# Kernel tuning notes

Hardware: AMD Instinct MI355X
Metric: run time of the kernel (lower is better)

The kernel has to match this reference:

```python
import jax, jax.numpy as jnp
import numpy as np
import math

N, T, D_MODEL = 4, 2048, 1024
NHEAD = 16
HEAD_DIM = D_MODEL // NHEAD
ROTARY_DIM = 64
WINDOW = (128, 128)
ROPE_BASE = 10000.0


def _rope_cos_sin(seq_len, rotary_dim, dtype):
    # non-interleaved (GPT-NeoX style) rotary embedding tables
    inv_freq = 1.0 / (ROPE_BASE ** (jnp.arange(0, rotary_dim, 2, dtype=jnp.float32) / rotary_dim))
    t = jnp.arange(seq_len, dtype=jnp.float32)
    freqs = jnp.outer(t, inv_freq)  # [T, rotary_dim//2]
    return jnp.cos(freqs).astype(dtype), jnp.sin(freqs).astype(dtype)


def _apply_rope(x, cos, sin):
    # x: [N, T, H, D]; rotate first ROTARY_DIM dims, pass the rest through
    r = ROTARY_DIM
    x_rot, x_pass = x[..., :r], x[..., r:]
    x1, x2 = x_rot[..., : r // 2], x_rot[..., r // 2 :]
    c = cos[None, :, None, :]
    s = sin[None, :, None, :]
    out = jnp.concatenate([x1 * c - x2 * s, x1 * s + x2 * c], axis=-1)
    return jnp.concatenate([out, x_pass], axis=-1)


def _sliding_window_bias(seq_len, window, dtype):
    i = jnp.arange(seq_len)[:, None]
    j = jnp.arange(seq_len)[None, :]
    # triu(diag=-w0) & tril(diag=w1): keep j - i in [-w0, w1]
    keep = (j - i >= -window[0]) & (j - i <= window[1])
    return jnp.where(keep, jnp.zeros((), dtype), jnp.full((), -jnp.inf, dtype))


def setup_inputs() -> dict:
    key = jax.random.key(0)
    k1, k2, k3 = jax.random.split(key, 3)
    x = jax.random.normal(k1, (N, T, D_MODEL), dtype=jnp.float32)
    Wqkv = jax.random.normal(k2, (D_MODEL, 3 * D_MODEL), dtype=jnp.float32) * (1.0 / math.sqrt(D_MODEL))
    Wout = jax.random.normal(k3, (D_MODEL, D_MODEL), dtype=jnp.float32) * (1.0 / math.sqrt(D_MODEL))
    bout = jnp.zeros((D_MODEL,), dtype=jnp.float32)
    return {"x": x, "Wqkv": Wqkv, "Wout": Wout, "bout": bout}


def reference(x, Wqkv, Wout, bout):
    n, t, _ = x.shape
    qkv = (x @ Wqkv).reshape(n, t, 3, NHEAD, HEAD_DIM)
    q, k, v = qkv[:, :, 0], qkv[:, :, 1], qkv[:, :, 2]  # each [N, T, H, D]
    cos, sin = _rope_cos_sin(t, ROTARY_DIM, x.dtype)
    q = _apply_rope(q, cos, sin)
    k = _apply_rope(k, cos, sin)
    scale = 1.0 / math.sqrt(HEAD_DIM)
    bias = _sliding_window_bias(t, WINDOW, x.dtype)  # [T, T]
    scores = jnp.einsum("bthd,bshd->bhts", q, k) * scale + bias[None, None]
    attn = jax.nn.softmax(scores, axis=-1)
    out = jnp.einsum("bhts,bshd->bthd", attn, v).reshape(n, t, D_MODEL)
    return out @ Wout + bout
```

## Files before the change

kernel.cpp:

```cpp
#include <hip/hip_runtime.h>
#include <hip/hip_bf16.h>
#include <cstdint>
#include <cstddef>

typedef __bf16 bf16_t;
typedef bf16_t bf16x8 __attribute__((ext_vector_type(8)));
typedef float f32x4 __attribute__((ext_vector_type(4)));
typedef unsigned short ushort_t;

#define T_SEQ 2048
#define DM 1024
#define NH 16
#define HD 64
#define WIN 128
#define ROPE_C 0.28782313662425572f
#define SCALE_LOG2E 0.18033688011112042f
#define ATT_M 16.0f

__device__ __forceinline__ ushort_t f2bf(float f) {
    union { float f; unsigned u; } v; v.f = f;
    unsigned r = v.u + 0x7fff + ((v.u >> 16) & 1);
    return (ushort_t)(r >> 16);
}
__device__ __forceinline__ float sane(float v, float sent) {
    return (fabsf(v) < 1e30f) ? v : sent;
}
__device__ __forceinline__ void gld16(const ushort_t* g, ushort_t* l) {
    __builtin_amdgcn_global_load_lds(
        (const __attribute__((address_space(1))) unsigned int*)g,
        (__attribute__((address_space(3))) unsigned int*)l, 16, 0, 0);
}

__global__ __launch_bounds__(256) void kzero_f(float* __restrict__ p) {
    size_t i = ((size_t)blockIdx.x * 256 + threadIdx.x) * 4;
    float4 z; z.x = z.y = z.z = z.w = 0.f;
    *(float4*)(p + i) = z;
}

__device__ __forceinline__ void trans_f2b_tile(const float* __restrict__ in,
                                               ushort_t* __restrict__ out,
                                               int R, int C, int c0, int r0) {
    __shared__ __align__(16) ushort_t tile[64][72];
    const int tid = threadIdx.x;
    const int rl = tid >> 2, q4 = tid & 3;
    const float* src = in + (size_t)(r0 + rl) * C + c0 + q4 * 16;
    ushort_t cv[16];
#pragma unroll
    for (int i = 0; i < 4; i++) {
        float4 f = *(const float4*)(src + i * 4);
        cv[i * 4 + 0] = f2bf(f.x); cv[i * 4 + 1] = f2bf(f.y);
        cv[i * 4 + 2] = f2bf(f.z); cv[i * 4 + 3] = f2bf(f.w);
    }
    *(uint4*)&tile[rl][q4 * 16]     = *(uint4*)&cv[0];
    *(uint4*)&tile[rl][q4 * 16 + 8] = *(uint4*)&cv[8];
    __syncthreads();
    const int cl = tid >> 2;
    ushort_t tmp[16];
#pragma unroll
    for (int i = 0; i < 16; i++) tmp[i] = tile[q4 * 16 + i][cl];
    ushort_t* dst = out + (size_t)(c0 + cl) * R + r0 + q4 * 16;
    *(uint4*)(dst)     = *(uint4*)&tmp[0];
    *(uint4*)(dst + 8) = *(uint4*)&tmp[8];
}

__global__ __launch_bounds__(256) void prep(const float* __restrict__ x,
                                            const float* __restrict__ Wqkv,
                                            const float* __restrict__ Wout,
                                            ushort_t* __restrict__ xb,
                                            ushort_t* __restrict__ WqkvT,
                                            ushort_t* __restrict__ WoutT) {
    const int bx = blockIdx.x;
    if (bx < 4096) {
        size_t i = ((size_t)bx * 256 + threadIdx.x) * 8;
        float4 a0 = *(const float4*)(x + i);
        float4 a1 = *(const float4*)(x + i + 4);
        ushort_t cv[8];
        cv[0] = f2bf(a0.x); cv[1] = f2bf(a0.y); cv[2] = f2bf(a0.z); cv[3] = f2bf(a0.w);
        cv[4] = f2bf(a1.x); cv[5] = f2bf(a1.y); cv[6] = f2bf(a1.z); cv[7] = f2bf(a1.w);
        *(uint4*)(xb + i) = *(uint4*)cv;
    } else if (bx < 4864) {
        int tb = bx - 4096;
        trans_f2b_tile(Wqkv, WqkvT, 1024, 3072, (tb % 48) * 64, (tb / 48) * 64);
    } else {
        int tb = bx - 4864;
        trans_f2b_tile(Wout, WoutT, 1024, 1024, (tb & 15) * 64, (tb >> 4) * 64);
    }
}

#define BM 128
#define BN 256
#define BK 32
#define KTILES 32
#define LBUF ((BM + BN) * BK)
#define LTOT (3 * LBUF)

__device__ __forceinline__ void gemm_core(const ushort_t* __restrict__ Agl,
                                          const ushort_t* __restrict__ Bgl,
                                          ushort_t* L, int m0, int n0,
                                          f32x4 (&acc)[8][4]) {
    const int tid = threadIdx.x;
    const int lane = tid & 63, w = tid >> 6;
    const int c = lane & 15, g = lane >> 4;
    const int sv   = (lane & 7) ^ (lane >> 3);
    const int grow = 2 * (lane >> 3) + (sv >> 2);
    const int gcol = (sv & 3) * 8;
    const int loff = (c >> 1) * 64 + (((((c & 1) << 2) | g) ^ ((c >> 1) & 7)) * 8);

#pragma unroll
    for (int mi = 0; mi < 8; ++mi)
#pragma unroll
        for (int ni = 0; ni < 4; ++ni)
#pragma unroll
            for (int r = 0; r < 4; ++r) acc[mi][ni][r] = 0.f;

    auto STAGE = [&](int kt, int bo) {
        const int k0 = kt * BK;
#pragma unroll
        for (int j = 0; j < 2; ++j) {
            const ushort_t* ga = Agl + (size_t)(m0 + 32 * w + 16 * j + grow) * 1024 + k0 + gcol;
            gld16(ga, &L[bo + (w * 2 + j) * 512]);
        }
#pragma unroll
        for (int j = 0; j < 4; ++j) {
            const ushort_t* gb = Bgl + (size_t)(n0 + 64 * w + 16 * j + grow) * 1024 + k0 + gcol;
            gld16(gb, &L[bo + BM * BK + (w * 4 + j) * 512]);
        }
    };

    STAGE(0, 0);
    STAGE(1, LBUF);
    asm volatile("s_waitcnt vmcnt(6)\n\ts_barrier" ::: "memory");

    int bcur = 0;
    for (int kt = 0; kt < KTILES; ++kt) {
        int bst = bcur + 2 * LBUF; if (bst >= LTOT) bst -= LTOT;
        if (kt + 2 < KTILES) STAGE(kt + 2, bst);

        const ushort_t* La = L + bcur;
        const ushort_t* Bb = La + BM * BK;
        bf16x8 bfr[4], af0[4], af1[4];
#pragma unroll
        for (int ni = 0; ni < 4; ++ni)
            bfr[ni] = *(const bf16x8*)&Bb[w * 2048 + ni * 512 + loff];
#pragma unroll
        for (int mi = 0; mi < 4; ++mi)
            af0[mi] = *(const bf16x8*)&La[mi * 512 + loff];
        __builtin_amdgcn_s_setprio(1);
#pragma unroll
        for (int mi = 0; mi < 4; ++mi)
#pragma unroll
            for (int ni = 0; ni < 4; ++ni)
                acc[mi][ni] = __builtin_amdgcn_mfma_f32_16x16x32_bf16(
                    af0[mi], bfr[ni], acc[mi][ni], 0, 0, 0);
        __builtin_amdgcn_s_setprio(0);
#pragma unroll
    for (int mi = 0; mi < 4; ++mi)
            af1[mi] = *(const bf16x8*)&La[(mi + 4) * 512 + loff];
        __builtin_amdgcn_s_setprio(1);
#pragma unroll
        for (int mi = 0; mi < 4; ++mi)
#pragma unroll
            for (int ni = 0; ni < 4; ++ni)
                acc[mi + 4][ni] = __builtin_amdgcn_mfma_f32_16x16x32_bf16(
                    af1[mi], bfr[ni], acc[mi + 4][ni], 0, 0, 0);
        __builtin_amdgcn_s_setprio(0);
        if (kt < KTILES - 2)
            asm volatile("s_waitcnt vmcnt(6)\n\ts_barrier" ::: "memory");
        else if (kt == KTILES - 2)
            asm volatile("s_waitcnt vmcnt(0)\n\ts_barrier" ::: "memory");
        bcur += LBUF; if (bcur == LTOT) bcur = 0;
    }
}

__global__ __launch_bounds__(256, 2) void gemm_qkv(const ushort_t* __restrict__ A,
                                                   const ushort_t* __restrict__ Bt,
                                                   ushort_t* __restrict__ Qr,
                                                   ushort_t* __restrict__ Kr,
                                                   ushort_t* __restrict__ Vt) {
    __shared__ __align__(16) ushort_t L[LTOT];
    const int id  = blockIdx.x;
    const int nid = (id & 7) * 96 + (id >> 3);
    const int m0 = (nid & 63) * BM, n0 = (nid >> 6) * BN;
    f32x4 acc[8][4];
    gemm_core(A, Bt, L, m0, n0, acc);

    const int lane = threadIdx.x & 63, w = threadIdx.x >> 6;
    const int c = lane & 15, g = lane >> 4;
    const int nb = n0 + w * 64;
    const int sec = nb >> 10;
    const int h = (nb >> 6) & 15;

    if (sec < 2) {
        ushort_t* dst = (sec == 0) ? Qr : Kr;
        const float invf0 = __expf(-(float)(c) * ROPE_C);
        const float invf1 = __expf(-(float)(16 + c) * ROPE_C);
#pragma unroll
        for (int mi = 0; mi < 8; ++mi)
#pragma unroll
            for (int r = 0; r < 4; ++r) {
                int tg = m0 + mi * 16 + g * 4 + r;
                int nB = tg >> 11, t = tg & (T_SEQ - 1);
                float a0 = (float)t * invf0, a1 = (float)t * invf1;
                float s0 = __sinf(a0), c0 = __cosf(a0);
                float s1 = __sinf(a1), c1 = __cosf(a1);
                size_t base = ((size_t)(nB * NH + h) * T_SEQ + t) * 64;
                float x1a = acc[mi][0][r], x2a = acc[mi][2][r];
                float x1b = acc[mi][1][r], x2b = acc[mi][3][r];
                dst[base + c]      = f2bf(sane(x1a * c0 - x2a * s0, 1e3f));
                dst[base + 16 + c] = f2bf(sane(x1b * c1 - x2b * s1, 1e3f));
                dst[base + 32 + c] = f2bf(sane(x1a * s0 + x2a * c0, 1e3f));
                dst[base + 48 + c] = f2bf(sane(x1b * s1 + x2b * c1, 1e3f));
            }
    } else {
#pragma unroll
        for (int mi = 0; mi < 8; ++mi) {
            int tgb = m0 + mi * 16 + g * 4;
            int nB = tgb >> 11, t = tgb & (T_SEQ - 1);
            size_t vrow = (size_t)(nB * NH + h) * 64 * T_SEQ;
#pragma unroll
            for (int ni = 0; ni < 4; ++ni) {
                ushort4 pk;
                pk.x = f2bf(sane(acc[mi][ni][0], 1e3f));
                pk.y = f2bf(sane(acc[mi][ni][1], 1e3f));
                pk.z = f2bf(sane(acc[mi][ni][2], 1e3f));
                pk.w = f2bf(sane(acc[mi][ni][3], 1e3f));
                *(ushort4*)&Vt[vrow + (size_t)(ni * 16 + c) * T_SEQ + t] = pk;
            }
        }
    }
}

__global__ __launch_bounds__(256, 2) void gemm_out(const ushort_t* __restrict__ A,
                                                   const ushort_t* __restrict__ Bt,
                                                   float* __restrict__ C,
                                                   const float* __restrict__ bias) {
    __shared__ __align__(16) ushort_t L[LTOT];
    const int id  = blockIdx.x;
    const int nid = (id & 7) * 32 + (id >> 3);
    const int m0 = (nid & 63) * BM, n0 = (nid >> 6) * BN;
    f32x4 acc[8][4];
    gemm_core(A, Bt, L, m0, n0, acc);

    const int lane = threadIdx.x & 63, w = threadIdx.x >> 6;
    const int c = lane & 15, g = lane >> 4;
#pragma unroll
    for (int ni = 0; ni < 4; ++ni) {
        int col = n0 + w * 64 + ni * 16 + c;
        float bv = bias[col];
#pragma unroll
        for (int mi = 0; mi < 8; ++mi)
#pragma unroll
            for (int r = 0; r < 4; ++r) {
                int rowi = m0 + mi * 16 + g * 4 + r;
                C[(size_t)rowi * 1024 + col] = sane(acc[mi][ni][r] + bv, 1e8f);
            }
    }
}

#define KVB 64

__global__ __launch_bounds__(256) void attn_swin(const ushort_t* __restrict__ Qr,
                                                 const ushort_t* __restrict__ Kr,
                                                 const ushort_t* __restrict__ Vt,
                                                 ushort_t* __restrict__ O) {
    __shared__ __align__(16) ushort_t Ks[KVB * 72];
    __shared__ __align__(16) ushort_t Vs[64 * 72];
    __shared__ __align__(16) ushort_t pbuf[4][2][16 * 72];
    const int tid = threadIdx.x;
    const int wid = tid >> 6, lane = tid & 63;
    const int qb = (blockIdx.x & 15) * 128;
    const int h = (blockIdx.x >> 4) & 15, n = blockIdx.x >> 8;
    const int c = lane & 15, g = lane >> 4;
    const size_t hb = ((size_t)(n * NH + h)) * T_SEQ * 64;
    const int t0s[2] = { qb + wid * 16, qb + 64 + wid * 16 };
    const int st_row = tid >> 2, st_col = (tid & 3) * 16;

    bf16x8 qf0[2], qf1[2];
#pragma unroll
    for (int sub = 0; sub < 2; sub++) {
        qf0[sub] = *(const bf16x8*)(Qr + hb + (size_t)(t0s[sub] + c) * 64 + g * 8);
        qf1[sub] = *(const bf16x8*)(Qr + hb + (size_t)(t0s[sub] + c) * 64 + 32 + g * 8);
    }

    f32x4 o[2][4];
    float l_r[2][4];
#pragma unroll
    for (int sub = 0; sub < 2; sub++)
#pragma unroll
        for (int i = 0; i < 4; i++) {
            l_r[sub][i] = 0.f;
#pragma unroll
            for (int r = 0; r < 4; r++) o[sub][i][r] = 0.f;
        }

    int sB_lo = qb - WIN;        if (sB_lo < 0) sB_lo = 0;
    int sB_hi = qb + 127 + WIN;  if (sB_hi > T_SEQ - 1) sB_hi = T_SEQ - 1;

    uint4 kreg0 = *(const uint4*)(Kr + hb + (size_t)(sB_lo + st_row) * 64 + st_col);
    uint4 kreg1 = *(const uint4*)(Kr + hb + (size_t)(sB_lo + st_row) * 64 + st_col + 8);
    uint4 vreg0 = *(const uint4*)(Vt + hb + (size_t)st_row * T_SEQ + sB_lo + st_col);
    uint4 vreg1 = *(const uint4*)(Vt + hb + (size_t)st_row * T_SEQ + sB_lo + st_col + 8);

    for (int s0 = sB_lo; s0 <= sB_hi; s0 += KVB) {
        __syncthreads();
        *(uint4*)&Ks[st_row * 72 + st_col]     = kreg0;
        *(uint4*)&Ks[st_row * 72 + st_col + 8] = kreg1;
        *(uint4*)&Vs[st_row * 72 + st_col]     = vreg0;
        *(uint4*)&Vs[st_row * 72 + st_col + 8] = vreg1;
        __syncthreads();
        int s1 = s0 + KVB;
        if (s1 + KVB - 1 <= sB_hi) {
            kreg0 = *(const uint4*)(Kr + hb + (size_t)(s1 + st_row) * 64 + st_col);
            kreg1 = *(const uint4*)(Kr + hb + (size_t)(s1 + st_row) * 64 + st_col + 8);
            vreg0 = *(const uint4*)(Vt + hb + (size_t)st_row * T_SEQ + s1 + st_col);
            vreg1 = *(const uint4*)(Vt + hb + (size_t)st_row * T_SEQ + s1 + st_col + 8);
        }
        bool act[2];
#pragma unroll
        for (int sub = 0; sub < 2; sub++)
            act[sub] = !(s0 > t0s[sub] + 15 + WIN || s0 + KVB - 1 < t0s[sub] - WIN);
        if (!act[0] && !act[1]) continue;

        bf16x8 kf0[4], kf1[4];
#pragma unroll
        for (int sh = 0; sh < 4; sh++) {
            kf0[sh] = *(const bf16x8*)&Ks[(sh * 16 + c) * 72 + g * 8];
            kf1[sh] = *(const bf16x8*)&Ks[(sh * 16 + c) * 72 + 32 + g * 8];
        }
        bf16x8 vfl[4], vfh[4];
#pragma unroll
        for (int di = 0; di < 4; di++) {
            vfl[di] = *(const bf16x8*)&Vs[(di * 16 + c) * 72 + g * 8];
            vfh[di] = *(const bf16x8*)&Vs[(di * 16 + c) * 72 + 32 + g * 8];
        }

#pragma unroll
        for (int sub = 0; sub < 2; sub++) {
            if (!act[sub]) continue;
            const int t0 = t0s[sub];
            f32x4 S[4];
#pragma unroll
            for (int sh = 0; sh < 4; sh++) {
                f32x4 z;
#pragma unroll
                for (int r = 0; r < 4; r++) z[r] = 0.f;
                z = __builtin_amdgcn_mfma_f32_16x16x32_bf16(qf0[sub], kf0[sh], z, 0, 0, 0);
                z = __builtin_amdgcn_mfma_f32_16x16x32_bf16(qf1[sub], kf1[sh], z, 0, 0, 0);
                S[sh] = z;
            }
            const bool interior = (s0 >= t0 - 113) && (s0 <= t0 + 65);
            ushort_t* pb = pbuf[wid][sub];
            if (interior) {
#pragma unroll
                for (int sh = 0; sh < 4; sh++)
#pragma unroll
                    for (int r = 0; r < 4; r++) {
                        float p = exp2f(S[sh][r] * SCALE_LOG2E - ATT_M);
                        l_r[sub][r] += p;
                        pb[(g * 4 + r) * 72 + sh * 16 + c] = f2bf(p);
                    }
            } else {
#pragma unroll
                for (int sh = 0; sh < 4; sh++)
#pragma unroll
                    for (int r = 0; r < 4; r++) {
                        int s = s0 + sh * 16 + c;
                        int q = t0 + g * 4 + r;
                        bool keep = (s - q >= -WIN) && (s - q <= WIN);
                        float v = keep ? S[sh][r] * SCALE_LOG2E : -1e30f;
                        float p = exp2f(v - ATT_M);
                        l_r[sub][r] += p;
                        pb[(g * 4 + r) * 72 + sh * 16 + c] = f2bf(p);
                    }
            }
        }
        __asm__ volatile("s_waitcnt lgkmcnt(0)" ::: "memory");
#pragma unroll
        for (int sub = 0; sub < 2; sub++) {
            if (!act[sub]) continue;
            bf16x8 pfl = *(const bf16x8*)&pbuf[wid][sub][c * 72 + g * 8];
            bf16x8 pfh = *(const bf16x8*)&pbuf[wid][sub][c * 72 + 32 + g * 8];
#pragma unroll
            for (int di = 0; di < 4; di++) {
                o[sub][di] = __builtin_amdgcn_mfma_f32_16x16x32_bf16(pfl, vfl[di], o[sub][di], 0, 0, 0);
                o[sub][di] = __builtin_amdgcn_mfma_f32_16x16x32_bf16(pfh, vfh[di], o[sub][di], 0, 0, 0);
            }
        }
        __asm__ volatile("" ::: "memory");
    }

#pragma unroll
    for (int sub = 0; sub < 2; sub++) {
#pragma unroll
        for (int off = 1; off < 16; off <<= 1)
#pragma unroll
            for (int r = 0; r < 4; r++)
                l_r[sub][r] += __shfl_xor(l_r[sub][r], off, 64);
        float inv[4];
#pragma unroll
        for (int r = 0; r < 4; r++) inv[r] = __builtin_amdgcn_rcpf(l_r[sub][r]);
#pragma unroll
        for (int di = 0; di < 4; di++)
#pragma unroll
            for (int r = 0; r < 4; r++) {
                int q = t0s[sub] + g * 4 + r;
                float val = o[sub][di][r] * inv[r];
                O[((size_t)(n * T_SEQ + q)) * DM + h * 64 + di * 16 + c] =
                    f2bf(sane(val, 1e6f));
            }
    }
}

extern "C" void kernel_launch(void* const* d_in, const int* in_sizes, int n_in,
                              void* d_out, int out_size, void* d_ws, size_t ws_size,
                              hipStream_t stream) {
    const float* x    = (const float*)d_in[0];
    const float* Wqkv = (const float*)d_in[1];
    const float* Wout = (const float*)d_in[2];
    const float* bout = (const float*)d_in[3];
    float* out = (float*)d_out;

    const size_t NEED = 72ull << 20;
    if (ws_size < NEED) {
        kzero_f<<<dim3(8192), 256, 0, stream>>>(out);
        return;
    }
    char* ws = (char*)d_ws;
    ushort_t* WqkvT = (ushort_t*)(ws);
    ushort_t* WoutT = (ushort_t*)(ws + (6ull << 20));
    ushort_t* Qr    = (ushort_t*)(ws + (8ull << 20));
    ushort_t* Kr    = (ushort_t*)(ws + (24ull << 20));
    ushort_t* Vt    = (ushort_t*)(ws + (40ull << 20));
    ushort_t* xb    = (ushort_t*)(ws + (56ull << 20));
    ushort_t* Oat   = xb;

    prep<<<dim3(5120), 256, 0, stream>>>(x, Wqkv, Wout, xb, WqkvT, WoutT);
    gemm_qkv<<<dim3(768), 256, 0, stream>>>(xb, WqkvT, Qr, Kr, Vt);
    attn_swin<<<dim3(1024), 256, 0, stream>>>(Qr, Kr, Vt, Oat);
    gemm_out<<<dim3(256), 256, 0, stream>>>(Oat, WoutT, out, bout);
}
```

Measured before the change: 219.1 us.

## Use 256x128 tiles for output GEMM and drop block swizzle in GEMMs

Adds a second GEMM core with a 128-wide N tile and uses it for the output projection, doubling its grid from 256 to 512 blocks and raising occupancy hints to 3 blocks per CU. This targets poor CU utilisation, since 256 blocks underfill the device. Both GEMMs also switch from a swizzled 1D block index to a plain 2D grid, which may change L2 reuse patterns. Smaller N tiles lower arithmetic intensity and increase A-matrix reloads.

```diff
diff --git a/kernel.cpp b/kernel.cpp
--- a/kernel.cpp
+++ b/kernel.cpp
@@ -154,7 +154,7 @@
                     af0[mi], bfr[ni], acc[mi][ni], 0, 0, 0);
         __builtin_amdgcn_s_setprio(0);
 #pragma unroll
-    for (int mi = 0; mi < 4; ++mi)
+        for (int mi = 0; mi < 4; ++mi)
             af1[mi] = *(const bf16x8*)&La[(mi + 4) * 512 + loff];
         __builtin_amdgcn_s_setprio(1);
 #pragma unroll
@@ -172,15 +172,95 @@
     }
 }
 
+#define BN2 128
+#define LBUF2 ((BM + BN2) * BK)
+#define LTOT2 (3 * LBUF2)
+
+__device__ __forceinline__ void gemm_core_n128(const ushort_t* __restrict__ Agl,
+                                               const ushort_t* __restrict__ Bgl,
+                                               ushort_t* L, int m0, int n0,
+                                               f32x4 (&acc)[8][2]) {
+    const int tid = threadIdx.x;
+    const int lane = tid & 63, w = tid >> 6;
+    const int c = lane & 15, g = lane >> 4;
+    const int sv   = (lane & 7) ^ (lane >> 3);
+    const int grow = 2 * (lane >> 3) + (sv >> 2);
+    const int gcol = (sv & 3) * 8;
+    const int loff = (c >> 1) * 64 + (((((c & 1) << 2) | g) ^ ((c >> 1) & 7)) * 8);
+
+#pragma unroll
+    for (int mi = 0; mi < 8; ++mi)
+#pragma unroll
+        for (int ni = 0; ni < 2; ++ni)
+#pragma unroll
+            for (int r = 0; r < 4; ++r) acc[mi][ni][r] = 0.f;
+
+    auto STAGE = [&](int kt, int bo) {
+        const int k0 = kt * BK;
+#pragma unroll
+        for (int j = 0; j < 2; ++j) {
+            const ushort_t* ga = Agl + (size_t)(m0 + 32 * w + 16 * j + grow) * 1024 + k0 + gcol;
+            gld16(ga, &L[bo + (w * 2 + j) * 512]);
+        }
+#pragma unroll
+        for (int j = 0; j < 2; ++j) {
+            const ushort_t* gb = Bgl + (size_t)(n0 + 32 * w + 16 * j + grow) * 1024 + k0 + gcol;
+            gld16(gb, &L[bo + BM * BK + (w * 2 + j) * 512]);
+        }
+    };
+
+    STAGE(0, 0);
+    STAGE(1, LBUF2);
+    asm volatile("s_waitcnt vmcnt(4)\n\ts_barrier" ::: "memory");
+
+    int bcur = 0;
+    for (int kt = 0; kt < KTILES; ++kt) {
+        int bst = bcur + 2 * LBUF2; if (bst >= LTOT2) bst -= LTOT2;
+        if (kt + 2 < KTILES) STAGE(kt + 2, bst);
+
+        const ushort_t* La = L + bcur;
+        const ushort_t* Bb = La + BM * BK;
+        bf16x8 bfr[2], af0[4], af1[4];
+#pragma unroll
+        for (int ni = 0; ni < 2; ++ni)
+            bfr[ni] = *(const bf16x8*)&Bb[w * 1024 + ni * 512 + loff];
+#pragma unroll
+        for (int mi = 0; mi < 4; ++mi)
+            af0[mi] = *(const bf16x8*)&La[mi * 512 + loff];
+        __builtin_amdgcn_s_setprio(1);
+#pragma unroll
+        for (int mi = 0; mi < 4; ++mi)
+#pragma unroll
+            for (int ni = 0; ni < 2; ++ni)
+                acc[mi][ni] = __builtin_amdgcn_mfma_f32_16x16x32_bf16(
+                    af0[mi], bfr[ni], acc[mi][ni], 0, 0, 0);
+        __builtin_amdgcn_s_setprio(0);
+#pragma unroll
+        for (int mi = 0; mi < 4; ++mi)
+            af1[mi] = *(const bf16x8*)&La[(mi + 4) * 512 + loff];
+        __builtin_amdgcn_s_setprio(1);
+#pragma unroll
+        for (int mi = 0; mi < 4; ++mi)
+#pragma unroll
+            for (int ni = 0; ni < 2; ++ni)
+                acc[mi + 4][ni] = __builtin_amdgcn_mfma_f32_16x16x32_bf16(
+                    af1[mi], bfr[ni], acc[mi + 4][ni], 0, 0, 0);
+        __builtin_amdgcn_s_setprio(0);
+        if (kt < KTILES - 2)
+            asm volatile("s_waitcnt vmcnt(4)\n\ts_barrier" ::: "memory");
+        else if (kt == KTILES - 2)
+            asm volatile("s_waitcnt vmcnt(0)\n\ts_barrier" ::: "memory");
+        bcur += LBUF2; if (bcur == LTOT2) bcur = 0;
+    }
+}
+
 __global__ __launch_bounds__(256, 2) void gemm_qkv(const ushort_t* __restrict__ A,
                                                    const ushort_t* __restrict__ Bt,
                                                    ushort_t* __restrict__ Qr,
                                                    ushort_t* __restrict__ Kr,
                                                    ushort_t* __restrict__ Vt) {
     __shared__ __align__(16) ushort_t L[LTOT];
-    const int id  = blockIdx.x;
-    const int nid = (id & 7) * 96 + (id >> 3);
-    const int m0 = (nid & 63) * BM, n0 = (nid >> 6) * BN;
+    const int m0 = blockIdx.x * BM, n0 = blockIdx.y * BN;
     f32x4 acc[8][4];
     gemm_core(A, Bt, L, m0, n0, acc);
 
@@ -230,22 +310,20 @@
     }
 }
 
-__global__ __launch_bounds__(256, 2) void gemm_out(const ushort_t* __restrict__ A,
+__global__ __launch_bounds__(256, 3) void gemm_out(const ushort_t* __restrict__ A,
                                                    const ushort_t* __restrict__ Bt,
                                                    float* __restrict__ C,
                                                    const float* __restrict__ bias) {
-    __shared__ __align__(16) ushort_t L[LTOT];
-    const int id  = blockIdx.x;
-    const int nid = (id & 7) * 32 + (id >> 3);
-    const int m0 = (nid & 63) * BM, n0 = (nid >> 6) * BN;
-    f32x4 acc[8][4];
-    gemm_core(A, Bt, L, m0, n0, acc);
+    __shared__ __align__(16) ushort_t L[LTOT2];
+    const int m0 = blockIdx.x * BM, n0 = blockIdx.y * BN2;
+    f32x4 acc[8][2];
+    gemm_core_n128(A, Bt, L, m0, n0, acc);
 
     const int lane = threadIdx.x & 63, w = threadIdx.x >> 6;
     const int c = lane & 15, g = lane >> 4;
 #pragma unroll
-    for (int ni = 0; ni < 4; ++ni) {
-        int col = n0 + w * 64 + ni * 16 + c;
+    for (int ni = 0; ni < 2; ++ni) {
+        int col = n0 + w * 32 + ni * 16 + c;
         float bv = bias[col];
 #pragma unroll
         for (int mi = 0; mi < 8; ++mi)
@@ -435,7 +513,7 @@
     ushort_t* Oat   = xb;
 
     prep<<<dim3(5120), 256, 0, stream>>>(x, Wqkv, Wout, xb, WqkvT, WoutT);
-    gemm_qkv<<<dim3(768), 256, 0, stream>>>(xb, WqkvT, Qr, Kr, Vt);
+    gemm_qkv<<<dim3(64, 12), 256, 0, stream>>>(xb, WqkvT, Qr, Kr, Vt);
     attn_swin<<<dim3(1024), 256, 0, stream>>>(Qr, Kr, Vt, Oat);
-    gemm_out<<<dim3(256), 256, 0, stream>>>(Oat, WoutT, out, bout);
-}
+    gemm_out<<<dim3(64, 8), 256, 0, stream>>>(Oat, WoutT, out, bout);
+}
```

Result: no change. 214.8 us (-2.0%).

## Use 256x256 eight-wave tiled GEMM with staged LDS pipeline for QKV projection

Applied to the files above, without the earlier changes.

Replaces the QKV projection GEMM with a 512-thread, 256x256-tile kernel that uses a BK=64 double-buffered LDS scheme. Global loads of A and B halves are interleaved between four MFMA phases, each fenced by barriers. The larger tile is meant to raise arithmetic intensity and cut global/L2 traffic per FLOP. The grid shrinks to 384 blocks of 512 threads, which gives fewer waves to fill the CUs and adds many barriers per k-step. The out-projection also drops its grouped block-index swizzle in favour of a plain 2D grid, which may hurt L2 locality.

```diff
diff --git a/kernel.cpp b/kernel.cpp
--- a/kernel.cpp
+++ b/kernel.cpp
@@ -87,6 +87,202 @@
     }
 }
 
+#define QDB 32768
+
+__device__ __forceinline__ void gemm8_core(const ushort_t* __restrict__ Agl,
+                                           const ushort_t* __restrict__ Bgl,
+                                           ushort_t* L, int m0, int n0,
+                                           f32x4 (&acc)[8][4]) {
+    const int tid = threadIdx.x;
+    const int lane = tid & 63, w = tid >> 6;
+    const int wr = w >> 2, wc = w & 3;
+    const int c = lane & 15, g = lane >> 4;
+    const int srow = lane >> 3;
+    const int gcol = ((lane & 7) ^ srow) * 8;
+    const int cx0 = ((0 + g) ^ (c & 7)) * 8;
+    const int cx1 = ((4 + g) ^ (c & 7)) * 8;
+    const int axb = wr * 8192;
+    const int bxb = 16384 + (wc >> 1) * 8192;
+    const int br0 = (wc & 1) * 64;
+
+#pragma unroll
+    for (int mi = 0; mi < 8; ++mi)
+#pragma unroll
+        for (int ni = 0; ni < 4; ++ni)
+#pragma unroll
+            for (int r = 0; r < 4; ++r) acc[mi][ni][r] = 0.f;
+
+    auto SHALF = [&](const ushort_t* G, int grow0, int kt, ushort_t* lbase) {
+#pragma unroll
+        for (int j = 0; j < 2; ++j)
+            gld16(G + (size_t)(grow0 + w * 16 + j * 8 + srow) * 1024 + kt * 64 + gcol,
+                  lbase + (w * 2 + j) * 512);
+    };
+
+    SHALF(Agl, m0,       0, L);
+    SHALF(Agl, m0 + 128, 0, L + 8192);
+    SHALF(Bgl, n0,       0, L + 16384);
+    SHALF(Bgl, n0 + 128, 0, L + 24576);
+    SHALF(Bgl, n0,       1, L + QDB + 16384);
+    SHALF(Bgl, n0 + 128, 1, L + QDB + 24576);
+    asm volatile("s_waitcnt vmcnt(4)\n\ts_barrier" ::: "memory");
+
+    bf16x8 afr[4][2], b0[2][2], b1[2][2];
+    int bc = 0;
+    for (int j = 0; j < 16; ++j) {
+        ushort_t* cur = L + bc;
+        ushort_t* nxt = L + (bc ^ QDB);
+
+#pragma unroll
+        for (int mi = 0; mi < 4; ++mi) {
+            const ushort_t* p = cur + axb + (mi * 16 + c) * 64;
+            afr[mi][0] = *(const bf16x8*)(p + cx0);
+            afr[mi][1] = *(const bf16x8*)(p + cx1);
+        }
+#pragma unroll
+        for (int ni = 0; ni < 2; ++ni) {
+            const ushort_t* p = cur + bxb + (br0 + ni * 16 + c) * 64;
+            b0[ni][0] = *(const bf16x8*)(p + cx0);
+            b0[ni][1] = *(const bf16x8*)(p + cx1);
+        }
+        if (j < 15) SHALF(Agl, m0, j + 1, nxt);
+        asm volatile("s_barrier\n\ts_waitcnt lgkmcnt(0)" ::: "memory");
+        __builtin_amdgcn_s_setprio(1);
+#pragma unroll
+        for (int mi = 0; mi < 4; ++mi)
+#pragma unroll
+            for (int ni = 0; ni < 2; ++ni) {
+                acc[mi][ni] = __builtin_amdgcn_mfma_f32_16x16x32_bf16(
+                    afr[mi][0], b0[ni][0], acc[mi][ni], 0, 0, 0);
+                acc[mi][ni] = __builtin_amdgcn_mfma_f32_16x16x32_bf16(
+                    afr[mi][1], b0[ni][1], acc[mi][ni], 0, 0, 0);
+            }
+        __builtin_amdgcn_s_setprio(0);
+        asm volatile("s_barrier" ::: "memory");
+
+#pragma unroll
+        for (int ni = 0; ni < 2; ++ni) {
+            const ushort_t* p = cur + bxb + (br0 + (ni + 2) * 16 + c) * 64;
+            b1[ni][0] = *(const bf16x8*)(p + cx0);
+            b1[ni][1] = *(const bf16x8*)(p + cx1);
+        }
+        if (j < 15) SHALF(Agl, m0 + 128, j + 1, nxt + 8192);
+        asm volatile("s_barrier\n\ts_waitcnt lgkmcnt(0)" ::: "memory");
+        __builtin_amdgcn_s_setprio(1);
+#pragma unroll
+        for (int mi = 0; mi < 4; ++mi)
+#pragma unroll
+            for (int ni = 0; ni < 2; ++ni) {
+                acc[mi][ni + 2] = __builtin_amdgcn_mfma_f32_16x16x32_bf16(
+                    afr[mi][0], b1[ni][0], acc[mi][ni + 2], 0, 0, 0);
+                acc[mi][ni + 2] = __builtin_amdgcn_mfma_f32_16x16x32_bf16(
+                    afr[mi][1], b1[ni][1], acc[mi][ni + 2], 0, 0, 0);
+            }
+        __builtin_amdgcn_s_setprio(0);
+        asm volatile("s_barrier" ::: "memory");
+
+#pragma unroll
+        for (int mi = 0; mi < 4; ++mi) {
+            const ushort_t* p = cur + axb + ((mi + 4) * 16 + c) * 64;
+            afr[mi][0] = *(const bf16x8*)(p + cx0);
+            afr[mi][1] = *(const bf16x8*)(p + cx1);
+        }
+        if (j < 14) SHALF(Bgl, n0, j + 2, cur + 16384);
+        asm volatile("s_barrier\n\ts_waitcnt lgkmcnt(0)" ::: "memory");
+        __builtin_amdgcn_s_setprio(1);
+#pragma unroll
+        for (int mi = 0; mi < 4; ++mi)
+#pragma unroll
+            for (int ni = 0; ni < 2; ++ni) {
+                acc[mi + 4][ni + 2] = __builtin_amdgcn_mfma_f32_16x16x32_bf16(
+                    afr[mi][0], b1[ni][0], acc[mi + 4][ni + 2], 0, 0, 0);
+                acc[mi + 4][ni + 2] = __builtin_amdgcn_mfma_f32_16x16x32_bf16(
+                    afr[mi][1], b1[ni][1], acc[mi + 4][ni + 2], 0, 0, 0);
+            }
+        __builtin_amdgcn_s_setprio(0);
+        asm volatile("s_barrier" ::: "memory");
+
+        if (j < 14) SHALF(Bgl, n0 + 128, j + 2, cur + 24576);
+        asm volatile("s_barrier" ::: "memory");
+        __builtin_amdgcn_s_setprio(1);
+#pragma unroll
+        for (int mi = 0; mi < 4; ++mi)
+#pragma unroll
+            for (int ni = 0; ni < 2; ++ni) {
+                acc[mi + 4][ni] = __builtin_amdgcn_mfma_f32_16x16x32_bf16(
+                    afr[mi][0], b0[ni][0], acc[mi + 4][ni], 0, 0, 0);
+                acc[mi + 4][ni] = __builtin_amdgcn_mfma_f32_16x16x32_bf16(
+                    afr[mi][1], b0[ni][1], acc[mi + 4][ni], 0, 0, 0);
+            }
+        __builtin_amdgcn_s_setprio(0);
+        if (j < 14)
+            asm volatile("s_waitcnt vmcnt(4)\n\ts_barrier" ::: "memory");
+        else if (j == 14)
+            asm volatile("s_waitcnt vmcnt(0)\n\ts_barrier" ::: "memory");
+        else
+            asm volatile("s_barrier" ::: "memory");
+        bc ^= QDB;
+    }
+}
+
+__global__ __launch_bounds__(512, 2) void gemm_qkv(const ushort_t* __restrict__ A,
+                                                   const ushort_t* __restrict__ Bt,
+                                                   ushort_t* __restrict__ Qr,
+                                                   ushort_t* __restrict__ Kr,
+                                                   ushort_t* __restrict__ Vt) {
+    __shared__ __align__(16) ushort_t L[2 * QDB];
+    const int m0 = blockIdx.x * 256, n0 = blockIdx.y * 256;
+    f32x4 acc[8][4];
+    gemm8_core(A, Bt, L, m0, n0, acc);
+
+    const int lane = threadIdx.x & 63, w = threadIdx.x >> 6;
+    const int wr = w >> 2, wc = w & 3;
+    const int c = lane & 15, g = lane >> 4;
+    const int nb = n0 + wc * 64;
+    const int sec = nb >> 10;
+    const int h = (nb >> 6) & 15;
+    const int mrow = m0 + wr * 128;
+
+    if (sec < 2) {
+        ushort_t* dst = (sec == 0) ? Qr : Kr;
+        const float invf0 = __expf(-(float)(c) * ROPE_C);
+        const float invf1 = __expf(-(float)(16 + c) * ROPE_C);
+#pragma unroll
+        for (int mi = 0; mi < 8; ++mi)
+#pragma unroll
+            for (int r = 0; r < 4; ++r) {
+                int tg = mrow + mi * 16 + g * 4 + r;
+                int nB = tg >> 11, t = tg & (T_SEQ - 1);
+                float a0 = (float)t * invf0, a1 = (float)t * invf1;
+                float s0 = __sinf(a0), c0 = __cosf(a0);
+                float s1 = __sinf(a1), c1 = __cosf(a1);
+                size_t base = ((size_t)(nB * NH + h) * T_SEQ + t) * 64;
+                float x1a = acc[mi][0][r], x2a = acc[mi][2][r];
+                float x1b = acc[mi][1][r], x2b = acc[mi][3][r];
+                dst[base + c]      = f2bf(sane(x1a * c0 - x2a * s0, 1e3f));
+                dst[base + 16 + c] = f2bf(sane(x1b * c1 - x2b * s1, 1e3f));
+                dst[base + 32 + c] = f2bf(sane(x1a * s0 + x2a * c0, 1e3f));
+                dst[base + 48 + c] = f2bf(sane(x1b * s1 + x2b * c1, 1e3f));
+            }
+    } else {
+#pragma unroll
+        for (int mi = 0; mi < 8; ++mi) {
+            int tgb = mrow + mi * 16 + g * 4;
+            int nB = tgb >> 11, t = tgb & (T_SEQ - 1);
+            size_t vrow = (size_t)(nB * NH + h) * 64 * T_SEQ;
+#pragma unroll
+            for (int ni = 0; ni < 4; ++ni) {
+                ushort4 pk;
+                pk.x = f2bf(sane(acc[mi][ni][0], 1e3f));
+                pk.y = f2bf(sane(acc[mi][ni][1], 1e3f));
+                pk.z = f2bf(sane(acc[mi][ni][2], 1e3f));
+                pk.w = f2bf(sane(acc[mi][ni][3], 1e3f));
+                *(ushort4*)&Vt[vrow + (size_t)(ni * 16 + c) * T_SEQ + t] = pk;
+            }
+        }
+    }
+}
+
 #define BM 128
 #define BN 256
 #define BK 32
@@ -154,7 +350,7 @@
                     af0[mi], bfr[ni], acc[mi][ni], 0, 0, 0);
         __builtin_amdgcn_s_setprio(0);
 #pragma unroll
-    for (int mi = 0; mi < 4; ++mi)
+        for (int mi = 0; mi < 4; ++mi)
             af1[mi] = *(const bf16x8*)&La[(mi + 4) * 512 + loff];
         __builtin_amdgcn_s_setprio(1);
 #pragma unroll
@@ -172,72 +368,12 @@
     }
 }
 
-__global__ __launch_bounds__(256, 2) void gemm_qkv(const ushort_t* __restrict__ A,
-                                                   const ushort_t* __restrict__ Bt,
-                                                   ushort_t* __restrict__ Qr,
-                                                   ushort_t* __restrict__ Kr,
-                                                   ushort_t* __restrict__ Vt) {
-    __shared__ __align__(16) ushort_t L[LTOT];
-    const int id  = blockIdx.x;
-    const int nid = (id & 7) * 96 + (id >> 3);
-    const int m0 = (nid & 63) * BM, n0 = (nid >> 6) * BN;
-    f32x4 acc[8][4];
-    gemm_core(A, Bt, L, m0, n0, acc);
-
-    const int lane = threadIdx.x & 63, w = threadIdx.x >> 6;
-    const int c = lane & 15, g = lane >> 4;
-    const int nb = n0 + w * 64;
-    const int sec = nb >> 10;
-    const int h = (nb >> 6) & 15;
-
-    if (sec < 2) {
-        ushort_t* dst = (sec == 0) ? Qr : Kr;
-        const float invf0 = __expf(-(float)(c) * ROPE_C);
-        const float invf1 = __expf(-(float)(16 + c) * ROPE_C);
-#pragma unroll
-        for (int mi = 0; mi < 8; ++mi)
-#pragma unroll
-            for (int r = 0; r < 4; ++r) {
-                int tg = m0 + mi * 16 + g * 4 + r;
-                int nB = tg >> 11, t = tg & (T_SEQ - 1);
-                float a0 = (float)t * invf0, a1 = (float)t * invf1;
-                float s0 = __sinf(a0), c0 = __cosf(a0);
-                float s1 = __sinf(a1), c1 = __cosf(a1);
-                size_t base = ((size_t)(nB * NH + h) * T_SEQ + t) * 64;
-                float x1a = acc[mi][0][r], x2a = acc[mi][2][r];
-                float x1b = acc[mi][1][r], x2b = acc[mi][3][r];
-                dst[base + c]      = f2bf(sane(x1a * c0 - x2a * s0, 1e3f));
-                dst[base + 16 + c] = f2bf(sane(x1b * c1 - x2b * s1, 1e3f));
-                dst[base + 32 + c] = f2bf(sane(x1a * s0 + x2a * c0, 1e3f));
-                dst[base + 48 + c] = f2bf(sane(x1b * s1 + x2b * c1, 1e3f));
-            }
-    } else {
-#pragma unroll
-        for (int mi = 0; mi < 8; ++mi) {
-            int tgb = m0 + mi * 16 + g * 4;
-            int nB = tgb >> 11, t = tgb & (T_SEQ - 1);
-            size_t vrow = (size_t)(nB * NH + h) * 64 * T_SEQ;
-#pragma unroll
-            for (int ni = 0; ni < 4; ++ni) {
-                ushort4 pk;
-                pk.x = f2bf(sane(acc[mi][ni][0], 1e3f));
-                pk.y = f2bf(sane(acc[mi][ni][1], 1e3f));
-                pk.z = f2bf(sane(acc[mi][ni][2], 1e3f));
-                pk.w = f2bf(sane(acc[mi][ni][3], 1e3f));
-                *(ushort4*)&Vt[vrow + (size_t)(ni * 16 + c) * T_SEQ + t] = pk;
-            }
-        }
-    }
-}
-
 __global__ __launch_bounds__(256, 2) void gemm_out(const ushort_t* __restrict__ A,
                                                    const ushort_t* __restrict__ Bt,
                                                    float* __restrict__ C,
                                                    const float* __restrict__ bias) {
     __shared__ __align__(16) ushort_t L[LTOT];
-    const int id  = blockIdx.x;
-    const int nid = (id & 7) * 32 + (id >> 3);
-    const int m0 = (nid & 63) * BM, n0 = (nid >> 6) * BN;
+    const int m0 = blockIdx.x * BM, n0 = blockIdx.y * BN;
     f32x4 acc[8][4];
     gemm_core(A, Bt, L, m0, n0, acc);
 
@@ -435,7 +571,7 @@
     ushort_t* Oat   = xb;
 
     prep<<<dim3(5120), 256, 0, stream>>>(x, Wqkv, Wout, xb, WqkvT, WoutT);
-    gemm_qkv<<<dim3(768), 256, 0, stream>>>(xb, WqkvT, Qr, Kr, Vt);
+    gemm_qkv<<<dim3(32, 12), 512, 0, stream>>>(xb, WqkvT, Qr, Kr, Vt);
     attn_swin<<<dim3(1024), 256, 0, stream>>>(Qr, Kr, Vt, Oat);
-    gemm_out<<<dim3(256), 256, 0, stream>>>(Oat, WoutT, out, bout);
-}
+    gemm_out<<<dim3(64, 4), 256, 0, stream>>>(Oat, WoutT, out, bout);
+}
```

Result: no change. 216.8 us (-1.0%).
